# Performance work log

Hardware: AMD Instinct MI355X
Metric: run time of the kernel (lower is better)

## Reference

```python
import jax, jax.numpy as jnp
import numpy as np

EMBED_DIM = 1024
NUM_HEADS = 16
HEAD_DIM = EMBED_DIM // NUM_HEADS
SCALE = HEAD_DIM ** -0.5


def setup_inputs() -> dict:
    key = jax.random.key(0)
    ks = jax.random.split(key, 11)
    b, n, c = 2, 2048, EMBED_DIM
    # xavier_uniform bound for square [c, c] weight
    bound = float(np.sqrt(6.0 / (c + c)))
    def xavier(k):
        return jax.random.uniform(k, (c, c), jnp.float32, -bound, bound)
    return {
        "q": jax.random.normal(ks[0], (b, n, c), jnp.float32),
        "k": jax.random.normal(ks[1], (b, n, c), jnp.float32),
        "v": jax.random.normal(ks[2], (b, n, c), jnp.float32),
        "wq": xavier(ks[3]), "bq": jnp.zeros((c,), jnp.float32),
        "wk": xavier(ks[4]), "bk": jnp.zeros((c,), jnp.float32),
        "wv": xavier(ks[5]), "bv": jnp.zeros((c,), jnp.float32),
        "wo": xavier(ks[6]), "bo": jnp.zeros((c,), jnp.float32),
    }


def reference(q, k, v, wq, bq, wk, bk, wv, bv, wo, bo):
    b, n, c = q.shape
    h, d = NUM_HEADS, HEAD_DIM
    # linear projections (torch Linear: x @ W^T + b)
    qh = (q @ wq.T + bq).reshape(b, n, h, d).transpose(0, 2, 1, 3)  # b h n d
    kh = (k @ wk.T + bk).reshape(b, n, h, d).transpose(0, 2, 1, 3)
    vh = (v @ wv.T + bv).reshape(b, n, h, d).transpose(0, 2, 1, 3)
    dots = jnp.einsum('bhid,bhjd->bhij', qh, kh) * SCALE
    attn = jax.nn.softmax(dots, axis=-1)  # dropout p=0 -> identity
    out = jnp.einsum('bhij,bhjd->bhid', attn, vh)
    out = out.transpose(0, 2, 1, 3).reshape(b, n, c)
    return out @ wo.T + bo
```

## Files before the change

kernel.cpp:

```cpp
#include <hip/hip_runtime.h>


typedef float f32x4 __attribute__((ext_vector_type(4)));
typedef float f32x16 __attribute__((ext_vector_type(16)));
typedef __bf16 bf16x8 __attribute__((ext_vector_type(8)));

#define SEQ 2048
#define CH 1024
#define NH 16
#define HD 64
#define TOK 4096
#define QSCALE 0.18033688011112042f

__device__ __forceinline__ unsigned short f2b(float f) {
  unsigned int u = __float_as_uint(f);
  u = (u + 0x7FFFu + ((u >> 16) & 1u)) >> 16;
  return (unsigned short)u;
}

__device__ __forceinline__ float fexp2(float x) {
  float r;
  asm("v_exp_f32 %0, %1" : "=v"(r) : "v"(x));
  return r;
}

__device__ __forceinline__ unsigned int cvtpk(float lo, float hi) {
  unsigned int r;
  asm("v_cvt_pk_bf16_f32 %0, %1, %2" : "=v"(r) : "v"(lo), "v"(hi));
  return r;
}

__device__ __forceinline__ void gload16(const void* g, void* l) {
  __builtin_amdgcn_global_load_lds(
      (const __attribute__((address_space(1))) unsigned int*)g,
      (__attribute__((address_space(3))) unsigned int*)l, 16, 0, 0);
}

struct CvtArgs {
  const float* src[4];
  unsigned short* dst[4];
  int n4[4];
};

__global__ __launch_bounds__(256) void cvt_kernel(CvtArgs a) {
  const int s = blockIdx.y;
  const int n4 = a.n4[s];
  const float4* __restrict__ src = (const float4*)a.src[s];
  unsigned short* __restrict__ dst = a.dst[s];
  const int stride = gridDim.x * blockDim.x;
  for (int i = blockIdx.x * blockDim.x + threadIdx.x; i < n4; i += stride) {
    float4 w = src[i];
    ushort4 o;
    o.x = f2b(w.x); o.y = f2b(w.y); o.z = f2b(w.z); o.w = f2b(w.w);
    *(ushort4*)(dst + 4 * (size_t)i) = o;
  }
}

struct Proj3Args {
  const float* X[3];
  const unsigned short* W[3];
  const float* bias[3];
  unsigned short* outb[3];
  int mode[3];
};

__global__ __launch_bounds__(256, 4) void proj3_kernel(Proj3Args a) {
  constexpr int BUFB = 8192 + 4096;
  __shared__ __align__(16) unsigned char smem[3 * BUFB];
  const int z = blockIdx.z;
  const float* __restrict__ X = a.X[z];
  const unsigned short* __restrict__ W = a.W[z];
  const float* __restrict__ bias = a.bias[z];
  unsigned short* __restrict__ outb = a.outb[z];
  const int mode = a.mode[z];
  const int tid = threadIdx.x, wid = tid >> 6, lane = tid & 63;
  const int wm = wid >> 1, wn = wid & 1;
  const int mt = blockIdx.x, nt = blockIdx.y;
  const int l15 = lane & 15, l4 = lane >> 4;

  const float* Asrc = X + (size_t)(mt * 128 + (tid >> 1)) * CH + (tid & 1) * 16;
  const unsigned short* Bsrc = W + (size_t)(nt * 64 + (tid >> 2)) * CH + (tid & 3) * 8;
  unsigned char* const Adst0 = smem + tid * 32;
  unsigned char* const Bdst0 = smem + 8192 + tid * 16;

  float bvv[2];
#pragma unroll
  for (int nj = 0; nj < 2; ++nj)
    bvv[nj] = bias[nt * 64 + wn * 32 + nj * 16 + l15];

  f32x4 acc[4][2] = {};
  float4 a0[4], a1[4];

#define LOADA(SET, T)                                                        \
  {                                                                          \
    _Pragma("unroll") for (int j = 0; j < 4; ++j)                            \
        SET[j] = *(const float4*)(Asrc + (T) * 32 + 4 * j);                  \
  }
#define DMAB(T) gload16(Bsrc + (T) * 32, Bdst0 + ((T) % 3) * BUFB);
#define WRITEA(SET, T)                                                       \
  {                                                                          \
    unsigned int pk[8];                                                      \
    _Pragma("unroll") for (int j = 0; j < 4; ++j) {                          \
      pk[2 * j] = cvtpk(SET[j].x, SET[j].y);                                 \
      pk[2 * j + 1] = cvtpk(SET[j].z, SET[j].w);                             \
    }                                                                        \
    unsigned char* d = Adst0 + ((T) % 3) * BUFB;                             \
    *(uint4*)d = make_uint4(pk[0], pk[1], pk[2], pk[3]);                     \
    *(uint4*)(d + 16) = make_uint4(pk[4], pk[5], pk[6], pk[7]);              \
  }

  LOADA(a0, 0);
  DMAB(0);
  LOADA(a1, 1);
  DMAB(1);
  asm volatile("s_waitcnt vmcnt(6)" ::: "memory");
  WRITEA(a0, 0);
  LOADA(a0, 2);
  asm volatile("s_waitcnt vmcnt(5)" ::: "memory");
  WRITEA(a1, 1);

#define STEP(S, WSET, LSET)                                                  \
  {                                                                          \
    const int s_ = (S);                                                      \
    asm volatile("s_waitcnt lgkmcnt(0)" ::: "memory");                       \
    __builtin_amdgcn_s_barrier();                                            \
    __builtin_amdgcn_sched_barrier(0);                                       \
    if (s_ + 2 < 32) DMAB(s_ + 2);                                           \
    if (s_ + 3 < 32) LOADA(LSET, s_ + 3);                                    \
    if (s_ <= 28)                                                            \
      asm volatile("s_waitcnt vmcnt(5)" ::: "memory");                       \
    else if (s_ == 29)                                                       \
      asm volatile("s_waitcnt vmcnt(1)" ::: "memory");                       \
    else                                                                     \
      asm volatile("s_waitcnt vmcnt(0)" ::: "memory");                       \
    if (s_ + 2 < 32) WRITEA(WSET, s_ + 2);                                   \
    unsigned char* Al = smem + (s_ % 3) * BUFB;                              \
    unsigned char* Bl = Al + 8192;                                           \
    bf16x8 af[4], bfr[2];                                                    \
    _Pragma("unroll") for (int mi = 0; mi < 4; ++mi)                         \
        af[mi] = *(const bf16x8*)(Al + (wm * 64 + mi * 16 + l15) * 64 + l4 * 16); \
    _Pragma("unroll") for (int nj = 0; nj < 2; ++nj)                         \
        bfr[nj] = *(const bf16x8*)(Bl + (wn * 32 + nj * 16 + l15) * 64 + l4 * 16); \
    __builtin_amdgcn_s_setprio(1);                                           \
    _Pragma("unroll") for (int mi = 0; mi < 4; ++mi)                         \
        _Pragma("unroll") for (int nj = 0; nj < 2; ++nj)                     \
        acc[mi][nj] = __builtin_amdgcn_mfma_f32_16x16x32_bf16(af[mi], bfr[nj], \
                                                              acc[mi][nj], 0, 0, 0); \
    __builtin_amdgcn_s_setprio(0);                                           \
  }

  for (int s2 = 0; s2 < 32; s2 += 2) {
    STEP(s2, a0, a1);
    STEP(s2 + 1, a1, a0);
  }
#undef STEP
#undef LOADA
#undef DMAB
#undef WRITEA

  const int row0 = mt * 128 + wm * 64;
  const int col0 = nt * 64 + wn * 32;
#pragma unroll
  for (int nj = 0; nj < 2; ++nj) {
    const int col = col0 + nj * 16 + l15;
    const float bv = bvv[nj];
    const int h = col >> 6, d = col & 63;
    if (mode == 3) {
#pragma unroll
      for (int mi = 0; mi < 4; ++mi) {
        const int row = row0 + mi * 16 + l4 * 4;
        const int b = row >> 11, n = row & (SEQ - 1);
        ushort4 o;
        o.x = f2b(acc[mi][nj][0] + bv);
        o.y = f2b(acc[mi][nj][1] + bv);
        o.z = f2b(acc[mi][nj][2] + bv);
        o.w = f2b(acc[mi][nj][3] + bv);
        *(ushort4*)(outb + ((size_t)(b * NH + h) * HD + d) * SEQ + n) = o;
      }
    } else {
#pragma unroll
      for (int mi = 0; mi < 4; ++mi) {
#pragma unroll
        for (int r = 0; r < 4; ++r) {
          const int row = row0 + mi * 16 + l4 * 4 + r;
          float v = acc[mi][nj][r] + bv;
          if (mode == 0) v *= QSCALE;
          const int b = row >> 11, n = row & (SEQ - 1);
          outb[(((size_t)(b * NH + h) * SEQ + n) << 6) + d] = f2b(v);
        }
      }
    }
  }
}

__device__ __forceinline__ void projo_stage(
    const unsigned short* __restrict__ X, const unsigned short* __restrict__ W,
    int mt, int nt, int k0, unsigned char* buf, int wid, int lane) {
#pragma unroll
  for (int is = 0; is < 2; ++is) {
    const int p = (wid * 2 + is) * 1024 + lane * 16;
    gload16(X + (size_t)(mt * 128 + (p >> 6)) * CH + k0 + ((p & 63) >> 1),
            buf + (wid * 2 + is) * 1024);
  }
  {
    const int p = wid * 1024 + lane * 16;
    gload16(W + (size_t)(nt * 64 + (p >> 6)) * CH + k0 + ((p & 63) >> 1),
            buf + 8192 + wid * 1024);
  }
}

__global__ __launch_bounds__(256, 4) void projo_kernel(
    const unsigned short* __restrict__ X, const unsigned short* __restrict__ W,
    const float* __restrict__ bias, float* __restrict__ outf) {
  constexpr int BUFB = 8192 + 4096;
  __shared__ __align__(16) unsigned char smem[3 * BUFB];
  const int tid = threadIdx.x, wid = tid >> 6, lane = tid & 63;
  const int wm = wid >> 1, wn = wid & 1;
  const int mt = blockIdx.x, nt = blockIdx.y;
  const int l15 = lane & 15, l4 = lane >> 4;

  float bvv[2];
#pragma unroll
  for (int nj = 0; nj < 2; ++nj)
    bvv[nj] = bias[nt * 64 + wn * 32 + nj * 16 + l15];

  f32x4 acc[4][2] = {};

  projo_stage(X, W, mt, nt, 0, smem, wid, lane);
  projo_stage(X, W, mt, nt, 32, smem + BUFB, wid, lane);

  for (int s = 0; s < 32; ++s) {
    if (s < 31) asm volatile("s_waitcnt vmcnt(3)" ::: "memory");
    else        asm volatile("s_waitcnt vmcnt(0)" ::: "memory");
    __builtin_amdgcn_s_barrier();
    __builtin_amdgcn_sched_barrier(0);
    if (s + 2 < 32)
      projo_stage(X, W, mt, nt, (s + 2) * 32, smem + ((s + 2) % 3) * BUFB, wid, lane);

    unsigned char* Al = smem + (s % 3) * BUFB;
    unsigned char* Bl = Al + 8192;
    bf16x8 af[4], bfr[2];
#pragma unroll
    for (int mi = 0; mi < 4; ++mi)
      af[mi] = *(const bf16x8*)(Al + (wm * 64 + mi * 16 + l15) * 64 + l4 * 16);
#pragma unroll
    for (int nj = 0; nj < 2; ++nj)
      bfr[nj] = *(const bf16x8*)(Bl + (wn * 32 + nj * 16 + l15) * 64 + l4 * 16);
    __builtin_amdgcn_s_setprio(1);
#pragma unroll
    for (int mi = 0; mi < 4; ++mi)
#pragma unroll
      for (int nj = 0; nj < 2; ++nj)
        acc[mi][nj] = __builtin_amdgcn_mfma_f32_16x16x32_bf16(af[mi], bfr[nj], acc[mi][nj], 0, 0, 0);
    __builtin_amdgcn_s_setprio(0);
  }

  const int row0 = mt * 128 + wm * 64;
  const int col0 = nt * 64 + wn * 32;
#pragma unroll
  for (int nj = 0; nj < 2; ++nj) {
    const int col = col0 + nj * 16 + l15;
    const float bv = bvv[nj];
#pragma unroll
    for (int mi = 0; mi < 4; ++mi)
#pragma unroll
      for (int r = 0; r < 4; ++r)
        outf[(size_t)(row0 + mi * 16 + l4 * 4 + r) * CH + col] = acc[mi][nj][r] + bv;
  }
}

__device__ __forceinline__ void stage_kv(
    const unsigned short* __restrict__ Kb, const unsigned short* __restrict__ Vb,
    int j0, unsigned char* buf, int ws3, int lane) {
#pragma unroll
  for (int is = 0; is < 2; ++is) {
    const int p = ws3 * 2048 + is * 1024 + lane * 16;
    const int row = p >> 7;
    const int sw = ((p & 127) ^ ((row & 7) << 4)) >> 1;
    gload16(Kb + (size_t)(j0 + row) * HD + sw, buf + ws3 * 2048 + is * 1024);
    gload16(Vb + (size_t)row * SEQ + j0 + sw, buf + 8192 + ws3 * 2048 + is * 1024);
  }
}

__global__ __launch_bounds__(512, 4) void attn_kernel(
    const unsigned short* __restrict__ Qh, const unsigned short* __restrict__ Kh,
    const unsigned short* __restrict__ Vt, unsigned short* __restrict__ AO) {
  __shared__ __align__(16) unsigned char smem[81920];
  const int tid = threadIdx.x, wid = tid >> 6, lane = tid & 63;
  const int l31 = lane & 31, h = lane >> 5;
  const int grp = wid >> 2, wq = wid & 3;
  const int bid = blockIdx.x;
  const int swz = (bid & 7) * 64 + (bid >> 3);
  const int qt = swz & 15, bh = swz >> 4;

  const unsigned short* Qb = Qh + ((size_t)bh * SEQ + qt * 128) * HD;
  const unsigned short* Kb = Kh + (size_t)bh * SEQ * HD;
  const unsigned short* Vb = Vt + (size_t)bh * HD * SEQ;
  unsigned char* kvb = smem + grp * 32768;
  unsigned char* Qreg = smem + 65536;
  const int jbase = grp * 16;

#pragma unroll
  for (int is = 0; is < 4; ++is) {
    const int p = wq * 4096 + is * 1024 + lane * 16;
    const int row = p >> 7;
    const int sw = ((p & 127) ^ ((row & 7) << 4)) >> 1;
    gload16(Qb + (size_t)row * HD + sw, Qreg + wq * 4096 + is * 1024);
  }
  stage_kv(Kb, Vb, jbase * 64, kvb, wq, lane);
  asm volatile("s_waitcnt vmcnt(4)" ::: "memory");

  bf16x8 qf[4];
  const int qrow = wq * 32 + l31;
#pragma unroll
  for (int ks = 0; ks < 4; ++ks)
    qf[ks] = *(const bf16x8*)(Qreg + qrow * 128 +
                              ((ks * 32 + h * 16) ^ ((qrow & 7) << 4)));

  stage_kv(Kb, Vb, (jbase + 1) * 64, kvb + 16384, wq, lane);

  f32x16 O[2] = {};
  float m = -1e30f, l = 0.f;

  for (int it = 0; it < 16; ++it) {
    if (it < 15) asm volatile("s_waitcnt vmcnt(4)" ::: "memory");
    else         asm volatile("s_waitcnt vmcnt(0)" ::: "memory");
    __builtin_amdgcn_s_barrier();
    __builtin_amdgcn_sched_barrier(0);

    unsigned char* Kc = kvb + ((it & 1) << 14);
    unsigned char* Vc = Kc + 8192;

    f32x16 st[2] = {};
    __builtin_amdgcn_s_setprio(1);
#pragma unroll
    for (int kb = 0; kb < 2; ++kb) {
#pragma unroll
      for (int ks = 0; ks < 4; ++ks) {
        const int krow = kb * 32 + l31;
        const bf16x8 kf = *(const bf16x8*)(Kc + krow * 128 +
                                           ((ks * 32 + h * 16) ^ ((krow & 7) << 4)));
        st[kb] = __builtin_amdgcn_mfma_f32_32x32x16_bf16(kf, qf[ks], st[kb], 0, 0, 0);
      }
    }
    __builtin_amdgcn_s_setprio(0);

    float t[8];
#pragma unroll
    for (int i = 0; i < 8; ++i)
      t[i] = fmaxf(fmaxf(st[0][i], st[0][i + 8]), fmaxf(st[1][i], st[1][i + 8]));
#pragma unroll
    for (int i = 0; i < 4; ++i) t[i] = fmaxf(t[i], t[i + 4]);
    float pmax = fmaxf(fmaxf(t[0], t[1]), fmaxf(t[2], t[3]));
    pmax = fmaxf(pmax, __shfl_xor(pmax, 32));
    if (__any(pmax > m + 8.f)) {
      const float mnew = fmaxf(m, pmax);
      const float alpha = fexp2(m - mnew);
#pragma unroll
      for (int r = 0; r < 16; ++r) {
        const int qO = (r & 3) + 8 * (r >> 2) + 4 * h;
        const float aO = __shfl(alpha, qO);
        O[0][r] *= aO;
        O[1][r] *= aO;
      }
      l *= alpha;
      m = mnew;
    }
#pragma unroll
    for (int kb = 0; kb < 2; ++kb)
#pragma unroll
      for (int i = 0; i < 16; ++i) st[kb][i] = fexp2(st[kb][i] - m);
    float s[8];
#pragma unroll
    for (int i = 0; i < 8; ++i)
      s[i] = (st[0][i] + st[0][i + 8]) + (st[1][i] + st[1][i + 8]);
#pragma unroll
    for (int i = 0; i < 4; ++i) s[i] += s[i + 4];
    float rs = (s[0] + s[1]) + (s[2] + s[3]);
    rs += __shfl_xor(rs, 32);
    l += rs;

    unsigned int pk[2][8];
#pragma unroll
    for (int kb = 0; kb < 2; ++kb)
#pragma unroll
      for (int j = 0; j < 8; ++j)
        pk[kb][j] = cvtpk(st[kb][2 * j], st[kb][2 * j + 1]);

    __builtin_amdgcn_s_setprio(1);
#pragma unroll
    for (int kk = 0; kk < 4; ++kk) {
      const int kb = kk >> 1, j0 = (kk & 1) * 4;
      const unsigned int p0 = pk[kb][j0 + 0], p1 = pk[kb][j0 + 1];
      const unsigned int p2 = pk[kb][j0 + 2], p3 = pk[kb][j0 + 3];
      const unsigned int u0 = h ? p0 : p2;
      const unsigned int u1 = h ? p1 : p3;
      const unsigned int su0 = __shfl_xor(u0, 32);
      const unsigned int su1 = __shfl_xor(u1, 32);
      const unsigned int d0 = h ? su0 : p0;
      const unsigned int d1 = h ? su1 : p1;
      const unsigned int d2 = h ? p2 : su0;
      const unsigned int d3 = h ? p3 : su1;
      uint4 aw = make_uint4(d0, d1, d2, d3);
      const bf16x8 af = *(const bf16x8*)&aw;
#pragma unroll
      for (int db = 0; db < 2; ++db) {
        const int vrow = db * 32 + l31;
        const bf16x8 vf = *(const bf16x8*)(Vc + vrow * 128 +
                                           ((kk * 32 + h * 16) ^ ((vrow & 7) << 4)));
        O[db] = __builtin_amdgcn_mfma_f32_32x32x16_bf16(af, vf, O[db], 0, 0, 0);
      }
    }
    __builtin_amdgcn_s_setprio(0);

    __builtin_amdgcn_s_barrier();
    if (it + 2 < 16)
      stage_kv(Kb, Vb, (jbase + it + 2) * 64, Kc, wq, lane);
  }

  float2* slotO = (float2*)(smem + wq * 8960);
  float2* slotML = (float2*)(smem + wq * 8960 + 8704);
  if (grp == 1) {
    float2* dst = slotO + lane * 17;
#pragma unroll
    for (int i = 0; i < 8; ++i) dst[i] = make_float2(O[0][2 * i], O[0][2 * i + 1]);
#pragma unroll
    for (int i = 0; i < 8; ++i) dst[8 + i] = make_float2(O[1][2 * i], O[1][2 * i + 1]);
    if (h == 0) slotML[l31] = make_float2(m, l);
  }
  __builtin_amdgcn_s_barrier();
  if (grp == 0) {
    const float* src = (const float*)(slotO + lane * 17);
    const float2 ml1 = slotML[l31];
    const float mm = fmaxf(m, ml1.x);
    const float a0 = fexp2(m - mm), a1 = fexp2(ml1.x - mm);
    const float inv = 1.f / (a0 * l + a1 * ml1.y);
    const float w0 = a0 * inv, w1 = a1 * inv;
    const int b = bh >> 4, hh = bh & 15;
#pragma unroll
    for (int r = 0; r < 16; ++r) {
      const int qO = (r & 3) + 8 * (r >> 2) + 4 * h;
      const float s0 = __shfl(w0, qO), s1 = __shfl(w1, qO);
      const int n = qt * 128 + wq * 32 + qO;
      const size_t base = ((size_t)(b * SEQ + n)) * CH + hh * HD;
      AO[base + l31] = f2b(O[0][r] * s0 + src[r] * s1);
      AO[base + 32 + l31] = f2b(O[1][r] * s0 + src[16 + r] * s1);
    }
  }
}

extern "C" void kernel_launch(void* const* d_in, const int* in_sizes, int n_in,
                              void* d_out, int out_size, void* d_ws, size_t ws_size,
                              hipStream_t stream) {
  (void)in_sizes; (void)n_in; (void)out_size; (void)ws_size;
  const float* q  = (const float*)d_in[0];
  const float* k  = (const float*)d_in[1];
  const float* v  = (const float*)d_in[2];
  const float* wq = (const float*)d_in[3];
  const float* bq = (const float*)d_in[4];
  const float* wk = (const float*)d_in[5];
  const float* bk = (const float*)d_in[6];
  const float* wv = (const float*)d_in[7];
  const float* bv = (const float*)d_in[8];
  const float* wo = (const float*)d_in[9];
  const float* bo = (const float*)d_in[10];

  unsigned char* ws = (unsigned char*)d_ws;
  const size_t MB8 = 8u << 20;
  unsigned short* AO  = (unsigned short*)(ws + 0 * MB8);
  unsigned short* Vt  = (unsigned short*)(ws + 1 * MB8);
  unsigned short* wqb = (unsigned short*)(ws + 3 * MB8);
  unsigned short* wkb = (unsigned short*)(ws + 3 * MB8 + 1 * 2097152);
  unsigned short* wvb = (unsigned short*)(ws + 3 * MB8 + 2 * 2097152);
  unsigned short* wob = (unsigned short*)(ws + 3 * MB8 + 3 * 2097152);
  unsigned short* Qh  = (unsigned short*)(ws + 4 * MB8);
  unsigned short* Kh  = (unsigned short*)(ws + 5 * MB8);
  float* out = (float*)d_out;

  CvtArgs ca;
  ca.src[0] = wq; ca.dst[0] = wqb; ca.n4[0] = CH * CH / 4;
  ca.src[1] = wk; ca.dst[1] = wkb; ca.n4[1] = CH * CH / 4;
  ca.src[2] = wv; ca.dst[2] = wvb; ca.n4[2] = CH * CH / 4;
  ca.src[3] = wo; ca.dst[3] = wob; ca.n4[3] = CH * CH / 4;
  cvt_kernel<<<dim3(512, 4), 256, 0, stream>>>(ca);

  Proj3Args p3;
  p3.X[0] = q; p3.W[0] = wqb; p3.bias[0] = bq; p3.outb[0] = Qh; p3.mode[0] = 0;
  p3.X[1] = k; p3.W[1] = wkb; p3.bias[1] = bk; p3.outb[1] = Kh; p3.mode[1] = 1;
  p3.X[2] = v; p3.W[2] = wvb; p3.bias[2] = bv; p3.outb[2] = Vt; p3.mode[2] = 3;
  proj3_kernel<<<dim3(32, 16, 3), 256, 0, stream>>>(p3);

  attn_kernel<<<dim3(512), 512, 0, stream>>>(Qh, Kh, Vt, AO);

  projo_kernel<<<dim3(32, 16), 256, 0, stream>>>(AO, wob, bo, out);
}
```

Measured before the change: 144.6 us.

## Stage fp32 activations directly to LDS via async loads with swizzled layout

The projection GEMM now copies raw fp32 activation tiles straight into LDS with direct global-to-LDS loads, replacing the old path that went through registers with a bf16 convert before the LDS write. Conversion to bf16 moves to the point where each tile is read back from LDS, and an XOR swizzle is added to reduce bank conflicts. The pipeline changes from a 3-stage ring to double buffering with two barriers per step. The A tile doubles in LDS size and each wave now repeats the conversion work, which may cost occupancy or ALU time.

```diff
diff --git a/kernel.cpp b/kernel.cpp
--- a/kernel.cpp
+++ b/kernel.cpp
@@ -64,9 +64,28 @@
   int mode[3];
 };
 
+__device__ __forceinline__ void p3_stage(
+    const float* __restrict__ X, const unsigned short* __restrict__ W,
+    int mt, int nt, int k0, unsigned char* buf, int wid, int lane) {
+#pragma unroll
+  for (int is = 0; is < 4; ++is) {
+    const int p = wid * 4096 + is * 1024 + lane * 16;
+    const int row = p >> 7;
+    const int so = ((p & 127) ^ ((row & 7) << 4)) >> 2;
+    gload16(X + (size_t)(mt * 128 + row) * CH + k0 + so, buf + p);
+  }
+  {
+    const int p = wid * 1024 + lane * 16;
+    const int row = p >> 6;
+    const int so = ((p & 63) ^ ((row & 3) << 4)) >> 1;
+    gload16(W + (size_t)(nt * 64 + row) * CH + k0 + so, buf + 16384 + p);
+  }
+}
+
 __global__ __launch_bounds__(256, 4) void proj3_kernel(Proj3Args a) {
-  constexpr int BUFB = 8192 + 4096;
-  __shared__ __align__(16) unsigned char smem[3 * BUFB];
+  constexpr int ABYTES = 16384;
+  constexpr int BUFB = ABYTES + 4096;
+  __shared__ __align__(16) unsigned char smem[2 * BUFB];
   const int z = blockIdx.z;
   const float* __restrict__ X = a.X[z];
   const unsigned short* __restrict__ W = a.W[z];
@@ -78,85 +97,53 @@
   const int mt = blockIdx.x, nt = blockIdx.y;
   const int l15 = lane & 15, l4 = lane >> 4;
 
-  const float* Asrc = X + (size_t)(mt * 128 + (tid >> 1)) * CH + (tid & 1) * 16;
-  const unsigned short* Bsrc = W + (size_t)(nt * 64 + (tid >> 2)) * CH + (tid & 3) * 8;
-  unsigned char* const Adst0 = smem + tid * 32;
-  unsigned char* const Bdst0 = smem + 8192 + tid * 16;
-
   float bvv[2];
 #pragma unroll
   for (int nj = 0; nj < 2; ++nj)
     bvv[nj] = bias[nt * 64 + wn * 32 + nj * 16 + l15];
 
   f32x4 acc[4][2] = {};
-  float4 a0[4], a1[4];
-
-#define LOADA(SET, T)                                                        \
-  {                                                                          \
-    _Pragma("unroll") for (int j = 0; j < 4; ++j)                            \
-        SET[j] = *(const float4*)(Asrc + (T) * 32 + 4 * j);                  \
-  }
-#define DMAB(T) gload16(Bsrc + (T) * 32, Bdst0 + ((T) % 3) * BUFB);
-#define WRITEA(SET, T)                                                       \
-  {                                                                          \
-    unsigned int pk[8];                                                      \
-    _Pragma("unroll") for (int j = 0; j < 4; ++j) {                          \
-      pk[2 * j] = cvtpk(SET[j].x, SET[j].y);                                 \
-      pk[2 * j + 1] = cvtpk(SET[j].z, SET[j].w);                             \
-    }                                                                        \
-    unsigned char* d = Adst0 + ((T) % 3) * BUFB;                             \
-    *(uint4*)d = make_uint4(pk[0], pk[1], pk[2], pk[3]);                     \
-    *(uint4*)(d + 16) = make_uint4(pk[4], pk[5], pk[6], pk[7]);              \
-  }
-
-  LOADA(a0, 0);
-  DMAB(0);
-  LOADA(a1, 1);
-  DMAB(1);
-  asm volatile("s_waitcnt vmcnt(6)" ::: "memory");
-  WRITEA(a0, 0);
-  LOADA(a0, 2);
-  asm volatile("s_waitcnt vmcnt(5)" ::: "memory");
-  WRITEA(a1, 1);
-
-#define STEP(S, WSET, LSET)                                                  \
-  {                                                                          \
-    const int s_ = (S);                                                      \
-    asm volatile("s_waitcnt lgkmcnt(0)" ::: "memory");                       \
-    __builtin_amdgcn_s_barrier();                                            \
-    __builtin_amdgcn_sched_barrier(0);                                       \
-    if (s_ + 2 < 32) DMAB(s_ + 2);                                           \
-    if (s_ + 3 < 32) LOADA(LSET, s_ + 3);                                    \
-    if (s_ <= 28)                                                            \
-      asm volatile("s_waitcnt vmcnt(5)" ::: "memory");                       \
-    else if (s_ == 29)                                                       \
-      asm volatile("s_waitcnt vmcnt(1)" ::: "memory");                       \
-    else                                                                     \
-      asm volatile("s_waitcnt vmcnt(0)" ::: "memory");                       \
-    if (s_ + 2 < 32) WRITEA(WSET, s_ + 2);                                   \
-    unsigned char* Al = smem + (s_ % 3) * BUFB;                              \
-    unsigned char* Bl = Al + 8192;                                           \
-    bf16x8 af[4], bfr[2];                                                    \
-    _Pragma("unroll") for (int mi = 0; mi < 4; ++mi)                         \
-        af[mi] = *(const bf16x8*)(Al + (wm * 64 + mi * 16 + l15) * 64 + l4 * 16); \
-    _Pragma("unroll") for (int nj = 0; nj < 2; ++nj)                         \
-        bfr[nj] = *(const bf16x8*)(Bl + (wn * 32 + nj * 16 + l15) * 64 + l4 * 16); \
-    __builtin_amdgcn_s_setprio(1);                                           \
-    _Pragma("unroll") for (int mi = 0; mi < 4; ++mi)                         \
-        _Pragma("unroll") for (int nj = 0; nj < 2; ++nj)                     \
-        acc[mi][nj] = __builtin_amdgcn_mfma_f32_16x16x32_bf16(af[mi], bfr[nj], \
-                                                              acc[mi][nj], 0, 0, 0); \
-    __builtin_amdgcn_s_setprio(0);                                           \
-  }
-
-  for (int s2 = 0; s2 < 32; s2 += 2) {
-    STEP(s2, a0, a1);
-    STEP(s2 + 1, a1, a0);
-  }
-#undef STEP
-#undef LOADA
-#undef DMAB
-#undef WRITEA
+
+  p3_stage(X, W, mt, nt, 0, smem, wid, lane);
+  p3_stage(X, W, mt, nt, 32, smem + BUFB, wid, lane);
+
+  for (int s = 0; s < 32; ++s) {
+    if (s < 31) asm volatile("s_waitcnt vmcnt(5)" ::: "memory");
+    else        asm volatile("s_waitcnt vmcnt(0)" ::: "memory");
+    __builtin_amdgcn_s_barrier();
+    __builtin_amdgcn_sched_barrier(0);
+
+    unsigned char* Al = smem + (s & 1) * BUFB;
+    unsigned char* Bl = Al + ABYTES;
+
+    bf16x8 af[4], bfr[2];
+#pragma unroll
+    for (int mi = 0; mi < 4; ++mi) {
+      const int r = wm * 64 + mi * 16 + l15;
+      const int swz = (r & 7) << 4;
+      const f32x4 lo = *(const f32x4*)(Al + r * 128 + ((l4 * 32) ^ swz));
+      const f32x4 hi = *(const f32x4*)(Al + r * 128 + ((l4 * 32 + 16) ^ swz));
+      const uint4 aw = make_uint4(cvtpk(lo[0], lo[1]), cvtpk(lo[2], lo[3]),
+                                  cvtpk(hi[0], hi[1]), cvtpk(hi[2], hi[3]));
+      af[mi] = *(const bf16x8*)&aw;
+    }
+#pragma unroll
+    for (int nj = 0; nj < 2; ++nj) {
+      const int rb = wn * 32 + nj * 16 + l15;
+      bfr[nj] = *(const bf16x8*)(Bl + rb * 64 + ((l4 * 16) ^ ((rb & 3) << 4)));
+    }
+    __builtin_amdgcn_s_setprio(1);
+#pragma unroll
+    for (int mi = 0; mi < 4; ++mi)
+#pragma unroll
+      for (int nj = 0; nj < 2; ++nj)
+        acc[mi][nj] = __builtin_amdgcn_mfma_f32_16x16x32_bf16(af[mi], bfr[nj], acc[mi][nj], 0, 0, 0);
+    __builtin_amdgcn_s_setprio(0);
+
+    __builtin_amdgcn_s_barrier();
+    if (s + 2 < 32)
+      p3_stage(X, W, mt, nt, (s + 2) * 32, Al, wid, lane);
+  }
 
   const int row0 = mt * 128 + wm * 64;
   const int col0 = nt * 64 + wn * 32;
```

New measurement: 131.5 us. 9.1% less time.
